# Kernel tuning notes

Hardware: AMD Instinct MI355X
Metric: run time of the kernel (lower is better)

Reference implementation:

```python
import jax, jax.numpy as jnp
import numpy as np

H, N_EMB, D_EMB, D_UP = 1024, 8192, 512, 2048
B, T, BB, M, K_LABELS = 4, 4096, 512, 4096, 64


def _rms(x, w, eps=1e-6):
    xf = x.astype(jnp.float32)
    var = jnp.mean(xf * xf, axis=-1, keepdims=True)
    return (w * (xf * jax.lax.rsqrt(var + eps))).astype(x.dtype)


def setup_inputs() -> dict:
    key = jax.random.key(0)
    ks = jax.random.split(key, 8)
    bt = B * T
    inp = jax.random.normal(ks[0], (B, T, H), jnp.float32)
    w_k = jax.random.normal(ks[1], (N_EMB, H), jnp.float32) * 0.02
    w_v = jax.random.normal(ks[2], (N_EMB, D_EMB), jnp.float32) * 0.02
    w_up = jax.random.normal(ks[3], (D_UP, D_EMB), jnp.float32) * 0.02
    w_mix = jax.random.normal(ks[4], (H, D_UP + H), jnp.float32) * 0.02
    fw = jax.random.permutation(ks[5], bt)
    bw = jnp.argsort(fw)  # inverse permutation
    seq_sort = jax.random.randint(ks[6], (bt,), 0, K_LABELS)
    keep_cols = jnp.arange(M)  # keep first M of N_EMB rows
    emb_alloc = jnp.arange(N_EMB) % K_LABELS  # every label present among kept rows
    starts = jnp.zeros((bt,), jnp.int32)
    ends = jnp.full((bt,), M, jnp.int32)
    return {
        'input': inp, 'fw': fw, 'bw': bw, 'seq_sort': seq_sort,
        'keep_cols': keep_cols, 'emb_alloc': emb_alloc,
        'starts': starts, 'ends': ends, 'bb': BB,
        'w_k_weight': w_k, 'w_v_weight': w_v, 'w_up_weight': w_up,
        'w_mix_weight': w_mix,
        'norm_in_weight': jnp.ones((H,), jnp.float32),
        'norm_out_weight': jnp.ones((D_UP,), jnp.float32),
    }


def reference(input, fw, bw, seq_sort, keep_cols, emb_alloc, starts, ends, bb,
              w_k_weight, w_v_weight, w_up_weight, w_mix_weight,
              norm_in_weight, norm_out_weight):
    b, t, h = input.shape
    A = _rms(input, norm_in_weight)                      # [b,t,h]
    Bm = w_k_weight[keep_cols]                           # [m,h]
    Cm = w_v_weight[keep_cols]                           # [m,d_emb]
    la = emb_alloc[keep_cols]                            # [m]
    A = A.reshape(-1, h)[fw].reshape(-1, bb, h)          # [nb,bb,h]
    ss = seq_sort.reshape(-1, bb)                        # [nb,bb]
    st = starts.reshape(-1, bb).min(axis=-1)             # [nb]
    en = ends.reshape(-1, bb).max(axis=-1)               # [nb]
    # ragged per-block slice B[start:end] expressed as a kv range mask,
    # combined with the equality mask seq_sort[q] == emb_alloc[kv]
    scores = jnp.einsum('nqh,kh->nqk', A, Bm)            # [nb,bb,m]
    kv = jnp.arange(Bm.shape[0])
    mask = ((ss[:, :, None] == la[None, None, :])
            & (kv[None, None, :] >= st[:, None, None])
            & (kv[None, None, :] < en[:, None, None]))
    scores = jnp.where(mask, scores, -jnp.inf)
    p = jax.nn.softmax(scores, axis=-1)
    comb = jnp.einsum('nqk,kd->nqd', p, Cm)              # [nb,bb,d_emb]
    d_emb = Cm.shape[-1]
    comb = comb.reshape(-1, d_emb)[bw].reshape(b, t, d_emb)
    up = comb @ w_up_weight.T                            # [b,t,d_up]
    cat = jnp.concatenate([_rms(up, norm_out_weight), input], axis=-1)
    return cat @ w_mix_weight.T                          # [b,t,h]
```

## Files before the change

kernel.cpp:

```cpp
#include <hip/hip_runtime.h>
#include <hip/hip_bf16.h>
#include <cstdint>
#include <cstddef>

#define Hh 1024
#define D_EMB 512
#define D_UP 2048
#define BT 16384
#define BB_ 512
#define Mm 4096
#define NB 32
#define KL 64

typedef __attribute__((ext_vector_type(4))) float f4;
typedef __attribute__((ext_vector_type(4))) __bf16 bf4;
typedef __attribute__((ext_vector_type(8))) __bf16 bf8;
typedef __attribute__((ext_vector_type(4))) float f32x4;

__device__ __forceinline__ void gl_lds16(const void* g, void* l) {
  __builtin_amdgcn_global_load_lds((__attribute__((address_space(1))) void*)g,
                                   (__attribute__((address_space(3))) void*)l, 16, 0, 0);
}

__global__ __launch_bounds__(256) void conv_bf16_kernel(const float* __restrict__ src,
                                                        __bf16* __restrict__ dst, int n4) {
  int i = blockIdx.x * 256 + threadIdx.x;
  if (i >= n4) return;
  f4 v = ((const f4*)src)[i];
  bf4 o = {(__bf16)v[0], (__bf16)v[1], (__bf16)v[2], (__bf16)v[3]};
  ((bf4*)dst)[i] = o;
}

__global__ __launch_bounds__(256) void gather_bf16_kernel(const float* __restrict__ src,
                                                          const int* __restrict__ keep,
                                                          __bf16* __restrict__ dst, int cols4) {
  int row = blockIdx.x;
  const f4* s = (const f4*)src + (size_t)keep[row] * cols4;
  bf4* d = (bf4*)dst + (size_t)row * cols4;
  for (int i = threadIdx.x; i < cols4; i += 256) {
    f4 v = s[i];
    bf4 o = {(__bf16)v[0], (__bf16)v[1], (__bf16)v[2], (__bf16)v[3]};
    d[i] = o;
  }
}

__global__ __launch_bounds__(256) void la_kernel(const int* __restrict__ keep,
                                                 const int* __restrict__ emb,
                                                 int* __restrict__ la, int m) {
  int i = blockIdx.x * 256 + threadIdx.x;
  if (i < m) la[i] = emb[keep[i]];
}

__global__ __launch_bounds__(256) void range_kernel(const int* __restrict__ starts,
                                                    const int* __restrict__ ends,
                                                    int* __restrict__ stA, int* __restrict__ enA) {
  int n = blockIdx.x;
  int t = threadIdx.x, lane = t & 63, wv = t >> 6;
  int s1 = min(starts[n * BB_ + t], starts[n * BB_ + t + 256]);
  int e1 = max(ends[n * BB_ + t], ends[n * BB_ + t + 256]);
#pragma unroll
  for (int off = 32; off; off >>= 1) {
    s1 = min(s1, __shfl_xor(s1, off));
    e1 = max(e1, __shfl_xor(e1, off));
  }
  __shared__ int ssh[4], esh[4];
  if (lane == 0) { ssh[wv] = s1; esh[wv] = e1; }
  __syncthreads();
  if (t == 0) {
    int s = ssh[0], e = esh[0];
#pragma unroll
    for (int k = 1; k < 4; ++k) { s = min(s, ssh[k]); e = max(e, esh[k]); }
    stA[n] = s; enA[n] = e;
  }
}

__global__ __launch_bounds__(256) void qsort_kernel(const int* __restrict__ seq_sort,
                                                    int* __restrict__ qidx,
                                                    int* __restrict__ qoffA,
                                                    int* __restrict__ qcntA) {
  int n = blockIdx.x, tid = threadIdx.x;
  __shared__ int cnt[KL], pos[KL], pref[KL];
  if (tid < KL) cnt[tid] = 0;
  __syncthreads();
  int s0 = seq_sort[n * BB_ + tid];
  int s1 = seq_sort[n * BB_ + tid + 256];
  atomicAdd(&cnt[s0], 1);
  atomicAdd(&cnt[s1], 1);
  __syncthreads();
  if (tid == 0) {
    int a = 0;
    for (int s = 0; s < KL; ++s) { pref[s] = a; a += cnt[s]; }
  }
  __syncthreads();
  if (tid < KL) {
    pos[tid] = pref[tid];
    qoffA[n * KL + tid] = pref[tid];
    qcntA[n * KL + tid] = cnt[tid];
  }
  __syncthreads();
  int p0 = atomicAdd(&pos[s0], 1);
  qidx[n * BB_ + p0] = n * BB_ + tid;
  int p1 = atomicAdd(&pos[s1], 1);
  qidx[n * BB_ + p1] = n * BB_ + tid + 256;
}

__global__ __launch_bounds__(256) void ksort_kernel(const int* __restrict__ la,
                                                    const int* __restrict__ stA,
                                                    const int* __restrict__ enA,
                                                    int* __restrict__ kidx,
                                                    int* __restrict__ koffA,
                                                    int* __restrict__ kcntA) {
  int n = blockIdx.x, tid = threadIdx.x;
  int st = stA[n], en = enA[n];
  __shared__ int cnt[KL], pos[KL], pref[KL];
  if (tid < KL) cnt[tid] = 0;
  __syncthreads();
  for (int kv = st + tid; kv < en; kv += 256) atomicAdd(&cnt[la[kv]], 1);
  __syncthreads();
  if (tid == 0) {
    int a = 0;
    for (int s = 0; s < KL; ++s) { pref[s] = a; a += cnt[s]; }
  }
  __syncthreads();
  if (tid < KL) {
    pos[tid] = pref[tid];
    koffA[n * KL + tid] = pref[tid];
    kcntA[n * KL + tid] = cnt[tid];
  }
  __syncthreads();
  for (int kv = st + tid; kv < en; kv += 256) {
    int p = atomicAdd(&pos[la[kv]], 1);
    kidx[n * Mm + p] = kv;
  }
}

__global__ __launch_bounds__(256) void rms_in_kernel(const float* __restrict__ input,
                                                     const int* __restrict__ fw,
                                                     const float* __restrict__ wn,
                                                     __bf16* __restrict__ Aperm,
                                                     __bf16* __restrict__ inb) {
  int wv = threadIdx.x >> 6, lane = threadIdx.x & 63;
  int j = blockIdx.x * 4 + wv;
  {
    const f4* src = (const f4*)(input + (size_t)fw[j] * Hh);
    f4 v[4];
    float ss = 0.f;
#pragma unroll
    for (int c = 0; c < 4; ++c) {
      v[c] = src[c * 64 + lane];
      ss += v[c][0] * v[c][0] + v[c][1] * v[c][1] + v[c][2] * v[c][2] + v[c][3] * v[c][3];
    }
#pragma unroll
    for (int off = 32; off; off >>= 1) ss += __shfl_xor(ss, off);
    float sc = rsqrtf(ss * (1.f / Hh) + 1e-6f);
    const f4* w4 = (const f4*)wn;
    bf4* dst = (bf4*)(Aperm + (size_t)j * Hh);
#pragma unroll
    for (int c = 0; c < 4; ++c) {
      f4 w = w4[c * 64 + lane];
      bf4 o = {(__bf16)(v[c][0] * sc * w[0]), (__bf16)(v[c][1] * sc * w[1]),
               (__bf16)(v[c][2] * sc * w[2]), (__bf16)(v[c][3] * sc * w[3])};
      dst[c * 64 + lane] = o;
    }
  }
  {
    const f4* src = (const f4*)(input + (size_t)j * Hh);
    bf4* dst = (bf4*)(inb + (size_t)j * Hh);
#pragma unroll
    for (int c = 0; c < 4; ++c) {
      f4 t = src[c * 64 + lane];
      bf4 o = {(__bf16)t[0], (__bf16)t[1], (__bf16)t[2], (__bf16)t[3]};
      dst[c * 64 + lane] = o;
    }
  }
}

__global__ __launch_bounds__(256) void attn2_kernel(const __bf16* __restrict__ Aperm,
                                                    const __bf16* __restrict__ Bm,
                                                    const __bf16* __restrict__ Cm,
                                                    const int* __restrict__ qidx,
                                                    const int* __restrict__ qoffA,
                                                    const int* __restrict__ qcntA,
                                                    const int* __restrict__ kidx,
                                                    const int* __restrict__ koffA,
                                                    const int* __restrict__ kcntA,
                                                    const int* __restrict__ fw,
                                                    __bf16* __restrict__ comb) {
  int g = blockIdx.x;
  int n = g >> 6;
  int qcnt = qcntA[g];
  if (qcnt == 0) return;
  int kcnt = kcntA[g];
  int qbase = n * BB_ + qoffA[g];
  int kbase = n * Mm + koffA[g];
  int tid = threadIdx.x, lane = tid & 63, wv = tid >> 6;
  int c = lane & 15, rg = lane >> 4;
  __shared__ float Sbuf[16][66];

  for (int qt = 0; qt < qcnt; qt += 16) {
    int ql = qt + c;
    int j = qidx[qbase + (ql < qcnt ? ql : 0)];
    const __bf16* arow = Aperm + (size_t)j * Hh + rg * 8;

    float m[4] = {-1e30f, -1e30f, -1e30f, -1e30f};
    float l[4] = {0.f, 0.f, 0.f, 0.f};
    float acc[4][8];
#pragma unroll
    for (int r = 0; r < 4; ++r)
#pragma unroll
      for (int i = 0; i < 8; ++i) acc[r][i] = 0.f;

    int nch = (kcnt + 63) >> 6;
    for (int ch = 0; ch < nch; ++ch) {
      int posk = ch * 64 + wv * 16 + c;
      int kvr = (posk < kcnt) ? kidx[kbase + posk] : 0;
      const __bf16* brow = Bm + (size_t)kvr * Hh + rg * 8;
      f32x4 sacc = {0.f, 0.f, 0.f, 0.f};
#pragma unroll
      for (int ks = 0; ks < 32; ++ks) {
        bf8 af = *(const bf8*)(arow + ks * 32);
        bf8 bf_ = *(const bf8*)(brow + ks * 32);
        sacc = __builtin_amdgcn_mfma_f32_16x16x32_bf16(af, bf_, sacc, 0, 0, 0);
      }
      bool valid = posk < kcnt;
#pragma unroll
      for (int r = 0; r < 4; ++r) Sbuf[rg * 4 + r][wv * 16 + c] = valid ? sacc[r] : -1e30f;
      __syncthreads();

      int nval = min(64, kcnt - ch * 64);
      int kvl = (ch * 64 + lane < kcnt) ? kidx[kbase + ch * 64 + lane] : 0;
      float p[4];
#pragma unroll
      for (int r = 0; r < 4; ++r) {
        float s = Sbuf[wv * 4 + r][lane];
        float cm = s;
#pragma unroll
        for (int off = 32; off; off >>= 1) cm = fmaxf(cm, __shfl_xor(cm, off));
        float mn = fmaxf(m[r], cm);
        float sc = __expf(m[r] - mn);
        float pv = __expf(s - mn);
        float ssum = pv;
#pragma unroll
        for (int off = 32; off; off >>= 1) ssum += __shfl_xor(ssum, off);
        l[r] = l[r] * sc + ssum;
        m[r] = mn;
        p[r] = pv;
#pragma unroll
        for (int i = 0; i < 8; ++i) acc[r][i] *= sc;
      }
      for (int jj = 0; jj < nval; ++jj) {
        int kvr2 = __shfl(kvl, jj);
        bf8 v = *(const bf8*)(Cm + (size_t)kvr2 * D_EMB + lane * 8);
        float vf[8];
#pragma unroll
        for (int i = 0; i < 8; ++i) vf[i] = (float)v[i];
        float p0 = __shfl(p[0], jj), p1 = __shfl(p[1], jj);
        float p2 = __shfl(p[2], jj), p3 = __shfl(p[3], jj);
#pragma unroll
        for (int i = 0; i < 8; ++i) {
          acc[0][i] += p0 * vf[i];
          acc[1][i] += p1 * vf[i];
          acc[2][i] += p2 * vf[i];
          acc[3][i] += p3 * vf[i];
        }
      }
      __syncthreads();
    }
#pragma unroll
    for (int r = 0; r < 4; ++r) {
      int ql2 = qt + wv * 4 + r;
      if (ql2 < qcnt) {
        int j2 = qidx[qbase + ql2];
        float inv = 1.f / l[r];
        bf8 o;
#pragma unroll
        for (int i = 0; i < 8; ++i) o[i] = (__bf16)(acc[r][i] * inv);
        *(bf8*)(comb + (size_t)fw[j2] * D_EMB + lane * 8) = o;
      }
    }
  }
}

template <bool OUT_BF16>
__global__ __launch_bounds__(256, 2) void gemm_bt(const __bf16* __restrict__ x0, int k0,
                                                  const __bf16* __restrict__ x1, int k1,
                                                  const __bf16* __restrict__ w,
                                                  void* __restrict__ outp, int M, int N) {
  __shared__ __bf16 As[128 * 64];
  __shared__ __bf16 Bs[128 * 64];
  const int tid = threadIdx.x;
  const int lane = tid & 63, wv = tid >> 6;
  const int wr = wv >> 1, wc = wv & 1;
  const int m0 = blockIdx.y * 128, n0 = blockIdx.x * 128;
  const int K = k0 + k1;

  f32x4 zero = {0.f, 0.f, 0.f, 0.f};
  f32x4 acc[4][4];
#pragma unroll
  for (int a = 0; a < 4; ++a)
#pragma unroll
    for (int b = 0; b < 4; ++b) acc[a][b] = zero;

  for (int kb = 0; kb < K; kb += 64) {
    const __bf16* xs;
    int ld, kk;
    if (kb < k0) { xs = x0; ld = k0; kk = kb; }
    else         { xs = x1; ld = k1; kk = kb - k0; }
#pragma unroll
    for (int p = 0; p < 4; ++p) {
      int e = p * 256 + tid;
      int row = e >> 3, c8 = e & 7;
      gl_lds16(xs + (size_t)(m0 + row) * ld + kk + c8 * 8, (void*)(As + e * 8));
      gl_lds16(w + (size_t)(n0 + row) * K + kb + c8 * 8, (void*)(Bs + e * 8));
    }
    __syncthreads();
#pragma unroll
    for (int ks = 0; ks < 2; ++ks) {
      bf8 afr[4], bfr[4];
#pragma unroll
      for (int i = 0; i < 4; ++i) {
        afr[i] = *(const bf8*)(As + (wr * 64 + i * 16 + (lane & 15)) * 64 + ks * 32 + (lane >> 4) * 8);
        bfr[i] = *(const bf8*)(Bs + (wc * 64 + i * 16 + (lane & 15)) * 64 + ks * 32 + (lane >> 4) * 8);
      }
#pragma unroll
      for (int mi = 0; mi < 4; ++mi)
#pragma unroll
        for (int ni = 0; ni < 4; ++ni)
          acc[mi][ni] = __builtin_amdgcn_mfma_f32_16x16x32_bf16(afr[mi], bfr[ni], acc[mi][ni], 0, 0, 0);
    }
    __syncthreads();
  }
  const int r0 = (lane >> 4) * 4, cc = lane & 15;
#pragma unroll
  for (int mi = 0; mi < 4; ++mi) {
#pragma unroll
    for (int ni = 0; ni < 4; ++ni) {
      int col = n0 + wc * 64 + ni * 16 + cc;
#pragma unroll
      for (int r = 0; r < 4; ++r) {
        int row = m0 + wr * 64 + mi * 16 + r0 + r;
        float v = acc[mi][ni][r];
        if (OUT_BF16)
          ((__bf16*)outp)[(size_t)row * N + col] = (__bf16)v;
        else
          ((float*)outp)[(size_t)row * N + col] = v;
      }
    }
  }
}

__global__ __launch_bounds__(256) void rms_up_kernel(__bf16* __restrict__ up,
                                                     const float* __restrict__ wn) {
  int wv = threadIdx.x >> 6, lane = threadIdx.x & 63;
  size_t j = (size_t)blockIdx.x * 4 + wv;
  bf8* row = (bf8*)(up + j * D_UP);
  bf8 v[4];
  float ss = 0.f;
#pragma unroll
  for (int c = 0; c < 4; ++c) {
    v[c] = row[c * 64 + lane];
#pragma unroll
    for (int i = 0; i < 8; ++i) { float f = (float)v[c][i]; ss += f * f; }
  }
#pragma unroll
  for (int off = 32; off; off >>= 1) ss += __shfl_xor(ss, off);
  float sc = rsqrtf(ss * (1.f / D_UP) + 1e-6f);
#pragma unroll
  for (int c = 0; c < 4; ++c) {
    int ebase = (c * 64 + lane) * 8;
    f4 wa = *(const f4*)(wn + ebase);
    f4 wb = *(const f4*)(wn + ebase + 4);
    bf8 o;
#pragma unroll
    for (int i = 0; i < 4; ++i) o[i] = (__bf16)((float)v[c][i] * sc * wa[i]);
#pragma unroll
    for (int i = 0; i < 4; ++i) o[4 + i] = (__bf16)((float)v[c][4 + i] * sc * wb[i]);
    row[c * 64 + lane] = o;
  }
}

extern "C" void kernel_launch(void* const* d_in, const int* in_sizes, int n_in, void* d_out,
                              int out_size, void* d_ws, size_t ws_size, hipStream_t stream) {
  const float* input = (const float*)d_in[0];
  const int* fw = (const int*)d_in[1];
  const int* seq_sort = (const int*)d_in[3];
  const int* keep_cols = (const int*)d_in[4];
  const int* emb_alloc = (const int*)d_in[5];
  const int* starts = (const int*)d_in[6];
  const int* ends = (const int*)d_in[7];
  const float* w_k = (const float*)d_in[9];
  const float* w_v = (const float*)d_in[10];
  const float* w_up = (const float*)d_in[11];
  const float* w_mix = (const float*)d_in[12];
  const float* w_nin = (const float*)d_in[13];
  const float* w_nout = (const float*)d_in[14];

  char* p = (char*)d_ws;
  auto take = [&](size_t b) {
    void* r = (void*)p;
    p += (b + 255) & ~(size_t)255;
    return r;
  };
  __bf16* Aperm = (__bf16*)take((size_t)BT * Hh * 2);
  __bf16* inb = (__bf16*)take((size_t)BT * Hh * 2);
  __bf16* comb = (__bf16*)take((size_t)BT * D_EMB * 2);
  __bf16* up = (__bf16*)take((size_t)BT * D_UP * 2);
  __bf16* BmB = (__bf16*)take((size_t)Mm * Hh * 2);
  __bf16* CmB = (__bf16*)take((size_t)Mm * D_EMB * 2);
  __bf16* wupB = (__bf16*)take((size_t)D_UP * D_EMB * 2);
  __bf16* wmixB = (__bf16*)take((size_t)Hh * (D_UP + Hh) * 2);
  int* la = (int*)take(Mm * 4);
  int* stA = (int*)take(NB * 4);
  int* enA = (int*)take(NB * 4);
  int* qidx = (int*)take(BT * 4);
  int* qoffA = (int*)take(NB * KL * 4);
  int* qcntA = (int*)take(NB * KL * 4);
  int* kidx = (int*)take((size_t)NB * Mm * 4);
  int* koffA = (int*)take(NB * KL * 4);
  int* kcntA = (int*)take(NB * KL * 4);

  conv_bf16_kernel<<<(D_UP * D_EMB / 4 + 255) / 256, 256, 0, stream>>>(w_up, wupB, D_UP * D_EMB / 4);
  conv_bf16_kernel<<<(Hh * (D_UP + Hh) / 4 + 255) / 256, 256, 0, stream>>>(w_mix, wmixB,
                                                                           Hh * (D_UP + Hh) / 4);
  gather_bf16_kernel<<<Mm, 256, 0, stream>>>(w_k, keep_cols, BmB, Hh / 4);
  gather_bf16_kernel<<<Mm, 256, 0, stream>>>(w_v, keep_cols, CmB, D_EMB / 4);
  la_kernel<<<Mm / 256, 256, 0, stream>>>(keep_cols, emb_alloc, la, Mm);
  range_kernel<<<NB, 256, 0, stream>>>(starts, ends, stA, enA);
  qsort_kernel<<<NB, 256, 0, stream>>>(seq_sort, qidx, qoffA, qcntA);
  ksort_kernel<<<NB, 256, 0, stream>>>(la, stA, enA, kidx, koffA, kcntA);

  rms_in_kernel<<<BT / 4, 256, 0, stream>>>(input, fw, w_nin, Aperm, inb);
  attn2_kernel<<<NB * KL, 256, 0, stream>>>(Aperm, BmB, CmB, qidx, qoffA, qcntA, kidx, koffA,
                                            kcntA, fw, comb);
  gemm_bt<true><<<dim3(D_UP / 128, BT / 128), 256, 0, stream>>>(comb, D_EMB, (const __bf16*)nullptr,
                                                                0, wupB, (void*)up, BT, D_UP);
  rms_up_kernel<<<BT / 4, 256, 0, stream>>>(up, w_nout);
  gemm_bt<false><<<dim3(Hh / 128, BT / 128), 256, 0, stream>>>(up, D_UP, inb, Hh, wmixB, d_out, BT,
                                                               Hh);
}
```

Baseline: 404.1 us.

## Pre-sort keys by label and use MFMA for the P·V product in attention

Keys and values are regrouped once globally by label into contiguous buffers: K rows are gathered in sorted order and V is gathered and transposed into a padded layout. Each block's key range then comes from a binary search instead of a per-block index sort. The attention kernel reads contiguous K rows, and the probability-times-value product switches from scalar FMAs driven by shuffles to 16x16x32 bf16 MFMAs, with probabilities staged in LDS. This removes indirect loads and the scalar inner loop, at the cost of several small preprocessing kernels, bf16 rounding of the probabilities, and scattered 2-byte output stores.

```diff
diff --git a/kernel.cpp b/kernel.cpp
--- a/kernel.cpp
+++ b/kernel.cpp
@@ -9,6 +9,7 @@
 #define BT 16384
 #define BB_ 512
 #define Mm 4096
+#define MmP 4160
 #define NB 32
 #define KL 64
 
@@ -32,10 +33,10 @@
 }
 
 __global__ __launch_bounds__(256) void gather_bf16_kernel(const float* __restrict__ src,
-                                                          const int* __restrict__ keep,
+                                                          const int* __restrict__ idx,
                                                           __bf16* __restrict__ dst, int cols4) {
   int row = blockIdx.x;
-  const f4* s = (const f4*)src + (size_t)keep[row] * cols4;
+  const f4* s = (const f4*)src + (size_t)idx[row] * cols4;
   bf4* d = (bf4*)dst + (size_t)row * cols4;
   for (int i = threadIdx.x; i < cols4; i += 256) {
     f4 v = s[i];
@@ -74,6 +75,95 @@
   }
 }
 
+__global__ __launch_bounds__(256) void hist_kernel(const int* __restrict__ la,
+                                                   int* __restrict__ goff) {
+  __shared__ int cnt[KL];
+  int tid = threadIdx.x;
+  if (tid < KL) cnt[tid] = 0;
+  __syncthreads();
+  for (int k = tid; k < Mm; k += 256) atomicAdd(&cnt[la[k]], 1);
+  __syncthreads();
+  if (tid == 0) {
+    int a = 0;
+    for (int s = 0; s < KL; ++s) { goff[s] = a; a += cnt[s]; }
+    goff[KL] = a;
+  }
+}
+
+__global__ __launch_bounds__(256) void place_kernel(const int* __restrict__ la,
+                                                    const int* __restrict__ keep,
+                                                    const int* __restrict__ goff,
+                                                    int* __restrict__ gk,
+                                                    int* __restrict__ ridx) {
+  int s = blockIdx.x;
+  int tid = threadIdx.x, lane = tid & 63, wv = tid >> 6;
+  __shared__ int wc[4];
+  __shared__ int run;
+  if (tid == 0) run = goff[s];
+  __syncthreads();
+  for (int base = 0; base < Mm; base += 256) {
+    int k = base + tid;
+    bool f = (la[k] == s);
+    unsigned long long msk = __ballot(f);
+    int myidx = __popcll(msk & ((1ull << lane) - 1ull));
+    if (lane == 0) wc[wv] = __popcll(msk);
+    __syncthreads();
+    int woff = 0, tot = 0;
+#pragma unroll
+    for (int w = 0; w < 4; ++w) {
+      if (w < wv) woff += wc[w];
+      tot += wc[w];
+    }
+    int rbase = run;
+    if (f) {
+      int p = rbase + woff + myidx;
+      gk[p] = k;
+      ridx[p] = keep[k];
+    }
+    __syncthreads();
+    if (tid == 0) run = rbase + tot;
+    __syncthreads();
+  }
+}
+
+__global__ __launch_bounds__(256) void lohi_kernel(const int* __restrict__ gk,
+                                                   const int* __restrict__ goff,
+                                                   const int* __restrict__ stA,
+                                                   const int* __restrict__ enA,
+                                                   int* __restrict__ loA, int* __restrict__ hiA) {
+  int i = blockIdx.x * 256 + threadIdx.x;
+  if (i >= NB * KL) return;
+  int n = i / KL, s = i % KL;
+  int b = goff[s], e = goff[s + 1];
+  int st = stA[n], en = enA[n];
+  int lo = b, hi = e;
+  while (lo < hi) { int mid = (lo + hi) >> 1; if (gk[mid] < st) lo = mid + 1; else hi = mid; }
+  int L = lo;
+  lo = b; hi = e;
+  while (lo < hi) { int mid = (lo + hi) >> 1; if (gk[mid] < en) lo = mid + 1; else hi = mid; }
+  loA[i] = L;
+  hiA[i] = lo;
+}
+
+__global__ __launch_bounds__(256) void vt_kernel(const float* __restrict__ wv_,
+                                                 const int* __restrict__ ridx,
+                                                 __bf16* __restrict__ VT) {
+  int pb = blockIdx.x * 64;
+  int db = blockIdx.y * 64;
+  __shared__ float T[64][65];
+  int t = threadIdx.x;
+  int dl = t & 63, g = t >> 6;
+  for (int i = g * 16; i < g * 16 + 16; ++i) {
+    int r = ridx[pb + i];
+    T[dl][i] = wv_[(size_t)r * D_EMB + db + dl];
+  }
+  __syncthreads();
+  int pl = t & 63;
+  for (int j = g * 16; j < g * 16 + 16; ++j) {
+    VT[(size_t)(db + j) * MmP + pb + pl] = (__bf16)T[j][pl];
+  }
+}
+
 __global__ __launch_bounds__(256) void qsort_kernel(const int* __restrict__ seq_sort,
                                                     int* __restrict__ qidx,
                                                     int* __restrict__ qoffA,
@@ -102,36 +192,6 @@
   qidx[n * BB_ + p0] = n * BB_ + tid;
   int p1 = atomicAdd(&pos[s1], 1);
   qidx[n * BB_ + p1] = n * BB_ + tid + 256;
-}
-
-__global__ __launch_bounds__(256) void ksort_kernel(const int* __restrict__ la,
-                                                    const int* __restrict__ stA,
-                                                    const int* __restrict__ enA,
-                                                    int* __restrict__ kidx,
-                                                    int* __restrict__ koffA,
-                                                    int* __restrict__ kcntA) {
-  int n = blockIdx.x, tid = threadIdx.x;
-  int st = stA[n], en = enA[n];
-  __shared__ int cnt[KL], pos[KL], pref[KL];
-  if (tid < KL) cnt[tid] = 0;
-  __syncthreads();
-  for (int kv = st + tid; kv < en; kv += 256) atomicAdd(&cnt[la[kv]], 1);
-  __syncthreads();
-  if (tid == 0) {
-    int a = 0;
-    for (int s = 0; s < KL; ++s) { pref[s] = a; a += cnt[s]; }
-  }
-  __syncthreads();
-  if (tid < KL) {
-    pos[tid] = pref[tid];
-    koffA[n * KL + tid] = pref[tid];
-    kcntA[n * KL + tid] = cnt[tid];
-  }
-  __syncthreads();
-  for (int kv = st + tid; kv < en; kv += 256) {
-    int p = atomicAdd(&pos[la[kv]], 1);
-    kidx[n * Mm + p] = kv;
-  }
 }
 
 __global__ __launch_bounds__(256) void rms_in_kernel(const float* __restrict__ input,
@@ -175,27 +235,28 @@
   }
 }
 
-__global__ __launch_bounds__(256) void attn2_kernel(const __bf16* __restrict__ Aperm,
-                                                    const __bf16* __restrict__ Bm,
-                                                    const __bf16* __restrict__ Cm,
+__global__ __launch_bounds__(256) void attn3_kernel(const __bf16* __restrict__ Aperm,
+                                                    const __bf16* __restrict__ Ks,
+                                                    const __bf16* __restrict__ VT,
                                                     const int* __restrict__ qidx,
                                                     const int* __restrict__ qoffA,
                                                     const int* __restrict__ qcntA,
-                                                    const int* __restrict__ kidx,
-                                                    const int* __restrict__ koffA,
-                                                    const int* __restrict__ kcntA,
+                                                    const int* __restrict__ loA,
+                                                    const int* __restrict__ hiA,
                                                     const int* __restrict__ fw,
                                                     __bf16* __restrict__ comb) {
   int g = blockIdx.x;
-  int n = g >> 6;
   int qcnt = qcntA[g];
   if (qcnt == 0) return;
-  int kcnt = kcntA[g];
+  int n = g >> 6;
   int qbase = n * BB_ + qoffA[g];
-  int kbase = n * Mm + koffA[g];
+  int lo = loA[g], hi = hiA[g];
+  if (lo >= hi) return;
   int tid = threadIdx.x, lane = tid & 63, wv = tid >> 6;
   int c = lane & 15, rg = lane >> 4;
   __shared__ float Sbuf[16][66];
+  __shared__ __align__(16) __bf16 Plds[16][72];
+  __shared__ float scl[16], lrec[16];
 
   for (int qt = 0; qt < qcnt; qt += 16) {
     int ql = qt + c;
@@ -204,35 +265,30 @@
 
     float m[4] = {-1e30f, -1e30f, -1e30f, -1e30f};
     float l[4] = {0.f, 0.f, 0.f, 0.f};
-    float acc[4][8];
-#pragma unroll
-    for (int r = 0; r < 4; ++r)
-#pragma unroll
-      for (int i = 0; i < 8; ++i) acc[r][i] = 0.f;
-
-    int nch = (kcnt + 63) >> 6;
-    for (int ch = 0; ch < nch; ++ch) {
-      int posk = ch * 64 + wv * 16 + c;
-      int kvr = (posk < kcnt) ? kidx[kbase + posk] : 0;
-      const __bf16* brow = Bm + (size_t)kvr * Hh + rg * 8;
-      f32x4 sacc = {0.f, 0.f, 0.f, 0.f};
+    f32x4 acc[8];
+    f32x4 zero = {0.f, 0.f, 0.f, 0.f};
+#pragma unroll
+    for (int t8 = 0; t8 < 8; ++t8) acc[t8] = zero;
+
+    for (int p0 = lo; p0 < hi; p0 += 64) {
+      int kvcol = p0 + wv * 16 + c;
+      const __bf16* brow = Ks + (size_t)kvcol * Hh + rg * 8;
+      f32x4 sacc = zero;
 #pragma unroll
       for (int ks = 0; ks < 32; ++ks) {
         bf8 af = *(const bf8*)(arow + ks * 32);
         bf8 bf_ = *(const bf8*)(brow + ks * 32);
         sacc = __builtin_amdgcn_mfma_f32_16x16x32_bf16(af, bf_, sacc, 0, 0, 0);
       }
-      bool valid = posk < kcnt;
+      bool valid = kvcol < hi;
 #pragma unroll
       for (int r = 0; r < 4; ++r) Sbuf[rg * 4 + r][wv * 16 + c] = valid ? sacc[r] : -1e30f;
       __syncthreads();
 
-      int nval = min(64, kcnt - ch * 64);
-      int kvl = (ch * 64 + lane < kcnt) ? kidx[kbase + ch * 64 + lane] : 0;
-      float p[4];
 #pragma unroll
       for (int r = 0; r < 4; ++r) {
-        float s = Sbuf[wv * 4 + r][lane];
+        int q = wv * 4 + r;
+        float s = Sbuf[q][lane];
         float cm = s;
 #pragma unroll
         for (int off = 32; off; off >>= 1) cm = fmaxf(cm, __shfl_xor(cm, off));
@@ -244,40 +300,59 @@
         for (int off = 32; off; off >>= 1) ssum += __shfl_xor(ssum, off);
         l[r] = l[r] * sc + ssum;
         m[r] = mn;
-        p[r] = pv;
-#pragma unroll
-        for (int i = 0; i < 8; ++i) acc[r][i] *= sc;
-      }
-      for (int jj = 0; jj < nval; ++jj) {
-        int kvr2 = __shfl(kvl, jj);
-        bf8 v = *(const bf8*)(Cm + (size_t)kvr2 * D_EMB + lane * 8);
-        float vf[8];
-#pragma unroll
-        for (int i = 0; i < 8; ++i) vf[i] = (float)v[i];
-        float p0 = __shfl(p[0], jj), p1 = __shfl(p[1], jj);
-        float p2 = __shfl(p[2], jj), p3 = __shfl(p[3], jj);
-#pragma unroll
-        for (int i = 0; i < 8; ++i) {
-          acc[0][i] += p0 * vf[i];
-          acc[1][i] += p1 * vf[i];
-          acc[2][i] += p2 * vf[i];
-          acc[3][i] += p3 * vf[i];
-        }
+        Plds[q][lane] = (__bf16)pv;
+        if (lane == 0) scl[q] = sc;
       }
       __syncthreads();
-    }
+
+      float sf[4];
+#pragma unroll
+      for (int r = 0; r < 4; ++r) sf[r] = scl[rg * 4 + r];
+#pragma unroll
+      for (int t8 = 0; t8 < 8; ++t8)
+#pragma unroll
+        for (int r = 0; r < 4; ++r) acc[t8][r] *= sf[r];
+
+      bf8 pa0 = *(const bf8*)(&Plds[c][rg * 8]);
+      bf8 pa1 = *(const bf8*)(&Plds[c][32 + rg * 8]);
+#pragma unroll
+      for (int tt = 0; tt < 8; ++tt) {
+        int d = wv * 128 + tt * 16 + c;
+        const __bf16* vrow = VT + (size_t)d * MmP + p0 + rg * 8;
+        bf8 b0 = *(const bf8*)(vrow);
+        bf8 b1 = *(const bf8*)(vrow + 32);
+        acc[tt] = __builtin_amdgcn_mfma_f32_16x16x32_bf16(pa0, b0, acc[tt], 0, 0, 0);
+        acc[tt] = __builtin_amdgcn_mfma_f32_16x16x32_bf16(pa1, b1, acc[tt], 0, 0, 0);
+      }
+      __syncthreads();
+    }
+
+    if (lane == 0) {
+#pragma unroll
+      for (int r = 0; r < 4; ++r) lrec[wv * 4 + r] = l[r];
+    }
+    __syncthreads();
+    float inv[4];
+    size_t obase[4];
+    bool oval[4];
 #pragma unroll
     for (int r = 0; r < 4; ++r) {
-      int ql2 = qt + wv * 4 + r;
-      if (ql2 < qcnt) {
-        int j2 = qidx[qbase + ql2];
-        float inv = 1.f / l[r];
-        bf8 o;
-#pragma unroll
-        for (int i = 0; i < 8; ++i) o[i] = (__bf16)(acc[r][i] * inv);
-        *(bf8*)(comb + (size_t)fw[j2] * D_EMB + lane * 8) = o;
+      int qq = qt + rg * 4 + r;
+      oval[r] = qq < qcnt;
+      int j2 = qidx[qbase + (oval[r] ? qq : 0)];
+      obase[r] = (size_t)fw[j2] * D_EMB;
+      float lv = lrec[rg * 4 + r];
+      inv[r] = 1.f / lv;
+    }
+#pragma unroll
+    for (int tt = 0; tt < 8; ++tt) {
+      int d = wv * 128 + tt * 16 + c;
+#pragma unroll
+      for (int r = 0; r < 4; ++r) {
+        if (oval[r]) comb[obase[r] + d] = (__bf16)(acc[tt][r] * inv[r]);
       }
     }
+    __syncthreads();
   }
 }
 
@@ -405,33 +480,36 @@
   __bf16* inb = (__bf16*)take((size_t)BT * Hh * 2);
   __bf16* comb = (__bf16*)take((size_t)BT * D_EMB * 2);
   __bf16* up = (__bf16*)take((size_t)BT * D_UP * 2);
-  __bf16* BmB = (__bf16*)take((size_t)Mm * Hh * 2);
-  __bf16* CmB = (__bf16*)take((size_t)Mm * D_EMB * 2);
+  __bf16* Ks = (__bf16*)take((size_t)MmP * Hh * 2);
+  __bf16* VT = (__bf16*)take((size_t)D_EMB * MmP * 2);
   __bf16* wupB = (__bf16*)take((size_t)D_UP * D_EMB * 2);
   __bf16* wmixB = (__bf16*)take((size_t)Hh * (D_UP + Hh) * 2);
   int* la = (int*)take(Mm * 4);
   int* stA = (int*)take(NB * 4);
   int* enA = (int*)take(NB * 4);
+  int* goff = (int*)take((KL + 1) * 4);
+  int* gk = (int*)take(Mm * 4);
+  int* ridx = (int*)take(Mm * 4);
+  int* loA = (int*)take(NB * KL * 4);
+  int* hiA = (int*)take(NB * KL * 4);
   int* qidx = (int*)take(BT * 4);
   int* qoffA = (int*)take(NB * KL * 4);
   int* qcntA = (int*)take(NB * KL * 4);
-  int* kidx = (int*)take((size_t)NB * Mm * 4);
-  int* koffA = (int*)take(NB * KL * 4);
-  int* kcntA = (int*)take(NB * KL * 4);
 
   conv_bf16_kernel<<<(D_UP * D_EMB / 4 + 255) / 256, 256, 0, stream>>>(w_up, wupB, D_UP * D_EMB / 4);
   conv_bf16_kernel<<<(Hh * (D_UP + Hh) / 4 + 255) / 256, 256, 0, stream>>>(w_mix, wmixB,
                                                                            Hh * (D_UP + Hh) / 4);
-  gather_bf16_kernel<<<Mm, 256, 0, stream>>>(w_k, keep_cols, BmB, Hh / 4);
-  gather_bf16_kernel<<<Mm, 256, 0, stream>>>(w_v, keep_cols, CmB, D_EMB / 4);
   la_kernel<<<Mm / 256, 256, 0, stream>>>(keep_cols, emb_alloc, la, Mm);
   range_kernel<<<NB, 256, 0, stream>>>(starts, ends, stA, enA);
+  hist_kernel<<<1, 256, 0, stream>>>(la, goff);
+  place_kernel<<<KL, 256, 0, stream>>>(la, keep_cols, goff, gk, ridx);
+  lohi_kernel<<<(NB * KL + 255) / 256, 256, 0, stream>>>(gk, goff, stA, enA, loA, hiA);
+  gather_bf16_kernel<<<Mm, 256, 0, stream>>>(w_k, ridx, Ks, Hh / 4);
+  vt_kernel<<<dim3(Mm / 64, D_EMB / 64), 256, 0, stream>>>(w_v, ridx, VT);
   qsort_kernel<<<NB, 256, 0, stream>>>(seq_sort, qidx, qoffA, qcntA);
-  ksort_kernel<<<NB, 256, 0, stream>>>(la, stA, enA, kidx, koffA, kcntA);
 
   rms_in_kernel<<<BT / 4, 256, 0, stream>>>(input, fw, w_nin, Aperm, inb);
-  attn2_kernel<<<NB * KL, 256, 0, stream>>>(Aperm, BmB, CmB, qidx, qoffA, qcntA, kidx, koffA,
-                                            kcntA, fw, comb);
+  attn3_kernel<<<NB * KL, 256, 0, stream>>>(Aperm, Ks, VT, qidx, qoffA, qcntA, loA, hiA, fw, comb);
   gemm_bt<true><<<dim3(D_UP / 128, BT / 128), 256, 0, stream>>>(comb, D_EMB, (const __bf16*)nullptr,
                                                                 0, wupB, (void*)up, BT, D_UP);
   rms_up_kernel<<<BT / 4, 256, 0, stream>>>(up, w_nout);
```

New measurement: 364.8 us. -9.7%, faster.
